# Performance work log

Hardware: AMD Instinct MI355X
Metric: run time of the kernel (lower is better)

The kernel has to match this reference:

```python
import jax, jax.numpy as jnp
import numpy as np

B, L_SRC, L_TGT, H = 8, 256, 256, 768
N_SRC_WORDS, N_TGT_WORDS = 128, 128


def setup_inputs() -> dict:
    key = jax.random.key(0)
    k1, k2 = jax.random.split(key, 2)
    L = L_SRC + L_TGT
    tok_h = jax.random.normal(k1, (B, L, H), dtype=jnp.float32)
    attention_mask = jnp.ones((B, L), dtype=jnp.int32)
    # monotone word ids covering exactly N words (ragged spans of ~2 tokens/word)
    src_ids = (jnp.arange(L_SRC) * N_SRC_WORDS // L_SRC).astype(jnp.int64)
    tgt_ids = (jnp.arange(L_TGT) * N_TGT_WORDS // L_TGT).astype(jnp.int64)
    source_word_ids = jnp.broadcast_to(src_ids, (B, L_SRC))
    target_word_ids = jnp.broadcast_to(tgt_ids, (B, L_TGT))
    W = jax.random.normal(k2, (2 * H, 1), dtype=jnp.float32) * 0.02
    b = jnp.zeros((1,), dtype=jnp.float32)
    return dict(tok_h=tok_h, attention_mask=attention_mask,
                source_word_ids=source_word_ids, target_word_ids=target_word_ids,
                W=W, b=b, S=N_SRC_WORDS, T=N_TGT_WORDS)


def _pool_words(tok_h, combined_wid, attention_mask, n_words):
    """Vectorized equivalent of _pool_word_embeddings: mean over each
    contiguous run of equal word ids (masked / -1 tokens break runs)."""
    Bv, Lv, Hv = tok_h.shape
    valid = (attention_mask > 0) & (combined_wid >= 0)          # [B, L]
    prev_wid = jnp.pad(combined_wid[:, :-1], ((0, 0), (1, 0)), constant_values=-2)
    prev_valid = jnp.pad(valid[:, :-1], ((0, 0), (1, 0)), constant_values=False)
    new_run = valid & ((combined_wid != prev_wid) | (~prev_valid))
    run_id = jnp.cumsum(new_run.astype(jnp.int32), axis=1) - 1  # [B, L]
    n_seg = n_words + 1                                         # +1 dummy slot for invalid tokens
    seg = jnp.where(valid, run_id, n_words)
    gseg = (seg + jnp.arange(Bv, dtype=seg.dtype)[:, None] * n_seg).reshape(-1)
    sums = jax.ops.segment_sum(tok_h.reshape(Bv * Lv, Hv), gseg,
                               num_segments=Bv * n_seg).reshape(Bv, n_seg, Hv)
    counts = jax.ops.segment_sum(valid.astype(tok_h.dtype).reshape(-1), gseg,
                                 num_segments=Bv * n_seg).reshape(Bv, n_seg, 1)
    pooled = sums[:, :n_words] / jnp.maximum(counts[:, :n_words], 1.0)
    return pooled                                               # [B, n_words, H]


def reference(tok_h, attention_mask, source_word_ids, target_word_ids, W, b, S, T):
    combined_wid = jnp.concatenate([source_word_ids, target_word_ids], axis=1)  # [B, L]
    pooled = _pool_words(tok_h, combined_wid, attention_mask, S + T)            # [B, S+T, H]
    src = pooled[:, :S]            # [B, S, H]
    tgt = pooled[:, S:S + T]       # [B, T, H]
    # classifier(concat([src_exp, tgt_exp])) == src@W[:H] + tgt@W[H:] + b
    Hd = tok_h.shape[-1]
    w_src, w_tgt = W[:Hd, 0], W[Hd:, 0]
    logits = (src @ w_src)[:, :, None] + (tgt @ w_tgt)[:, None, :] + b[0]       # [B, S, T]
    return logits
```

## Files before the change

### kernel.cpp

```cpp
#include <hip/hip_runtime.h>
#include <hip/hip_bf16.h>

constexpr int B  = 8;
constexpr int LS = 256;
constexpr int L  = 512;
constexpr int H  = 768;
constexpr int S  = 128;
constexpr int NW = 256;

__global__ __launch_bounds__(256) void dot2_kernel(
    const float* __restrict__ tok, const float* __restrict__ Wp,
    float2* __restrict__ dvals)
{
    const int lane = threadIdx.x & 63;
    const int wv   = threadIdx.x >> 6;
    const int t0   = (blockIdx.x * 4 + wv) * 2;

    const float4* s4 = reinterpret_cast<const float4*>(Wp);
    const float4* g4 = reinterpret_cast<const float4*>(Wp + H);
    float4 wsv[3], wtv[3];
    #pragma unroll
    for (int k = 0; k < 3; ++k) {
        wsv[k] = s4[lane + 64 * k];
        wtv[k] = g4[lane + 64 * k];
    }

    const float4* ta = reinterpret_cast<const float4*>(tok + (size_t)t0 * H);
    const float4* tb = reinterpret_cast<const float4*>(tok + (size_t)(t0 + 1) * H);

    float as0 = 0.f, at0 = 0.f, as1 = 0.f, at1 = 0.f;
    #pragma unroll
    for (int k = 0; k < 3; ++k) {
        const float4 a = ta[lane + 64 * k];
        const float4 c = tb[lane + 64 * k];
        as0 += a.x * wsv[k].x + a.y * wsv[k].y + a.z * wsv[k].z + a.w * wsv[k].w;
        at0 += a.x * wtv[k].x + a.y * wtv[k].y + a.z * wtv[k].z + a.w * wtv[k].w;
        as1 += c.x * wsv[k].x + c.y * wsv[k].y + c.z * wsv[k].z + c.w * wsv[k].w;
        at1 += c.x * wtv[k].x + c.y * wtv[k].y + c.z * wtv[k].z + c.w * wtv[k].w;
    }
    #pragma unroll
    for (int off = 32; off; off >>= 1) {
        as0 += __shfl_xor(as0, off);
        at0 += __shfl_xor(at0, off);
        as1 += __shfl_xor(as1, off);
        at1 += __shfl_xor(at1, off);
    }
    if (lane == 0) {
        dvals[t0]     = make_float2(as0, at0);
        dvals[t0 + 1] = make_float2(as1, at1);
    }
}

__global__ __launch_bounds__(256) void finalize_kernel(
    const int* __restrict__ mask, const int* __restrict__ sw,
    const int* __restrict__ tw, const float2* __restrict__ dvals,
    const float* __restrict__ bias, float* __restrict__ out)
{
    const int g   = blockIdx.x;
    const int b   = g >> 4;
    const int sl  = g & 15;
    const int tid = threadIdx.x;

    __shared__ int   sseg[L];
    __shared__ float lsum[NW + 1];
    __shared__ float lcnt[NW + 1];
    __shared__ float pooled[NW];

    if (tid < NW + 1) { lsum[tid] = 0.f; lcnt[tid] = 0.f; }
    __syncthreads();

    if (tid < 64) {
        const int lane = tid;
        const int base = lane * 8;
        int wid[8]; bool val[8];
        #pragma unroll
        for (int j = 0; j < 8; ++j) {
            const int l = base + j;
            const int w = (l < LS) ? sw[b * LS + l] : tw[b * LS + (l - LS)];
            wid[j] = w;
            val[j] = (mask[b * L + l] > 0) && (w >= 0);
        }
        int pw = -2; bool pv = false;
        if (base > 0) {
            const int l = base - 1;
            pw = (l < LS) ? sw[b * LS + l] : tw[b * LS + (l - LS)];
            pv = (mask[b * L + l] > 0) && (pw >= 0);
        }
        int loc[8]; int c = 0;
        #pragma unroll
        for (int j = 0; j < 8; ++j) {
            const int nr = (val[j] && (wid[j] != pw || !pv)) ? 1 : 0;
            c += nr; loc[j] = c; pw = wid[j]; pv = val[j];
        }
        int inc = c;
        #pragma unroll
        for (int off = 1; off < 64; off <<= 1) {
            const int v = __shfl_up(inc, off);
            if (lane >= off) inc += v;
        }
        const int excl = inc - c;
        #pragma unroll
        for (int j = 0; j < 8; ++j) {
            const int rid = excl + loc[j] - 1;
            const int sg  = (val[j] && rid < NW) ? rid : NW;
            sseg[base + j] = sg;
        }
    }
    __syncthreads();

    #pragma unroll
    for (int r = 0; r < 2; ++r) {
        const int tl = tid + r * 256;
        const int sg = sseg[tl];
        atomicAdd(&lcnt[sg], 1.0f);
        if (sg < NW) {
            const float2 d = dvals[b * L + tl];
            atomicAdd(&lsum[sg], (sg < S) ? d.x : d.y);
        }
    }
    __syncthreads();

    if (tid < NW) pooled[tid] = lsum[tid] / fmaxf(lcnt[tid], 1.f);
    __syncthreads();

    const float b0 = bias[0];
    const int r = sl * 8 + (tid >> 5);
    const int c = (tid & 31) * 4;
    const float si = pooled[r] + b0;

    float4 v;
    v.x = si + pooled[S + c + 0];
    v.y = si + pooled[S + c + 1];
    v.z = si + pooled[S + c + 2];
    v.w = si + pooled[S + c + 3];
    *reinterpret_cast<float4*>(out + (size_t)b * S * 128 + r * 128 + c) = v;
}

extern "C" void kernel_launch(void* const* d_in, const int* in_sizes, int n_in,
                              void* d_out, int out_size, void* d_ws, size_t ws_size,
                              hipStream_t stream) {
    const float* tok  = (const float*)d_in[0];
    const int*   mask = (const int*)  d_in[1];
    const int*   sw   = (const int*)  d_in[2];
    const int*   tw   = (const int*)  d_in[3];
    const float* W    = (const float*)d_in[4];
    const float* bias = (const float*)d_in[5];
    float*       out  = (float*)d_out;

    float2* dvals = (float2*)d_ws;

    dot2_kernel<<<512, 256, 0, stream>>>(tok, W, dvals);
    finalize_kernel<<<128, 256, 0, stream>>>(mask, sw, tw, dvals, bias, out);
}
```

Measured before the change: 13.92 us.

## Use one token per wave in dot kernel and prefetch dvals into LDS

```diff
diff --git a/kernel.cpp b/kernel.cpp
--- a/kernel.cpp
+++ b/kernel.cpp
@@ -12,43 +12,29 @@
     const float* __restrict__ tok, const float* __restrict__ Wp,
     float2* __restrict__ dvals)
 {
-    const int lane = threadIdx.x & 63;
-    const int wv   = threadIdx.x >> 6;
-    const int t0   = (blockIdx.x * 4 + wv) * 2;
+    const int lane  = threadIdx.x & 63;
+    const int wv    = threadIdx.x >> 6;
+    const int token = blockIdx.x * 4 + wv;
 
     const float4* s4 = reinterpret_cast<const float4*>(Wp);
     const float4* g4 = reinterpret_cast<const float4*>(Wp + H);
-    float4 wsv[3], wtv[3];
+    const float4* t4 = reinterpret_cast<const float4*>(tok + (size_t)token * H);
+
+    float as = 0.f, at = 0.f;
     #pragma unroll
     for (int k = 0; k < 3; ++k) {
-        wsv[k] = s4[lane + 64 * k];
-        wtv[k] = g4[lane + 64 * k];
-    }
-
-    const float4* ta = reinterpret_cast<const float4*>(tok + (size_t)t0 * H);
-    const float4* tb = reinterpret_cast<const float4*>(tok + (size_t)(t0 + 1) * H);
-
-    float as0 = 0.f, at0 = 0.f, as1 = 0.f, at1 = 0.f;
-    #pragma unroll
-    for (int k = 0; k < 3; ++k) {
-        const float4 a = ta[lane + 64 * k];
-        const float4 c = tb[lane + 64 * k];
-        as0 += a.x * wsv[k].x + a.y * wsv[k].y + a.z * wsv[k].z + a.w * wsv[k].w;
-        at0 += a.x * wtv[k].x + a.y * wtv[k].y + a.z * wtv[k].z + a.w * wtv[k].w;
-        as1 += c.x * wsv[k].x + c.y * wsv[k].y + c.z * wsv[k].z + c.w * wsv[k].w;
-        at1 += c.x * wtv[k].x + c.y * wtv[k].y + c.z * wtv[k].z + c.w * wtv[k].w;
+        const float4 a = t4[lane + 64 * k];
+        const float4 s = s4[lane + 64 * k];
+        const float4 g = g4[lane + 64 * k];
+        as += a.x * s.x + a.y * s.y + a.z * s.z + a.w * s.w;
+        at += a.x * g.x + a.y * g.y + a.z * g.z + a.w * g.w;
     }
     #pragma unroll
     for (int off = 32; off; off >>= 1) {
-        as0 += __shfl_xor(as0, off);
-        at0 += __shfl_xor(at0, off);
-        as1 += __shfl_xor(as1, off);
-        at1 += __shfl_xor(at1, off);
+        as += __shfl_xor(as, off);
+        at += __shfl_xor(at, off);
     }
-    if (lane == 0) {
-        dvals[t0]     = make_float2(as0, at0);
-        dvals[t0 + 1] = make_float2(as1, at1);
-    }
+    if (lane == 0) dvals[token] = make_float2(as, at);
 }
 
 __global__ __launch_bounds__(256) void finalize_kernel(
@@ -61,13 +47,13 @@
     const int sl  = g & 15;
     const int tid = threadIdx.x;
 
-    __shared__ int   sseg[L];
-    __shared__ float lsum[NW + 1];
-    __shared__ float lcnt[NW + 1];
-    __shared__ float pooled[NW];
+    __shared__ int    sseg[L];
+    __shared__ float2 dv[L];
+    __shared__ float  lsum[NW + 1];
+    __shared__ float  lcnt[NW + 1];
+    __shared__ float  pooled[NW];
 
     if (tid < NW + 1) { lsum[tid] = 0.f; lcnt[tid] = 0.f; }
-    __syncthreads();
 
     if (tid < 64) {
         const int lane = tid;
@@ -105,6 +91,8 @@
             const int sg  = (val[j] && rid < NW) ? rid : NW;
             sseg[base + j] = sg;
         }
+    } else {
+        for (int i = tid - 64; i < L; i += 192) dv[i] = dvals[b * L + i];
     }
     __syncthreads();
 
@@ -114,7 +102,7 @@
         const int sg = sseg[tl];
         atomicAdd(&lcnt[sg], 1.0f);
         if (sg < NW) {
-            const float2 d = dvals[b * L + tl];
+            const float2 d = dv[tl];
             atomicAdd(&lsum[sg], (sg < S) ? d.x : d.y);
         }
     }
@@ -149,6 +137,6 @@
 
     float2* dvals = (float2*)d_ws;
 
-    dot2_kernel<<<512, 256, 0, stream>>>(tok, W, dvals);
+    dot2_kernel<<<1024, 256, 0, stream>>>(tok, W, dvals);
     finalize_kernel<<<128, 256, 0, stream>>>(mask, sw, tw, dvals, bias, out);
 }
```

After: 14.11 us. No clear change (+1.4%).
